# Kernel tuning notes

Measured on AMD Instinct MI355X. Metric: run time of the kernel, lower is better.

Reference implementation:

```python
import jax, jax.numpy as jnp
import numpy as np

B, T, D, F, C = 32768, 256, 10, 512, 1  # batch, trees, max_depth, features, classes
LVL_PAD = T * 2 ** (D - 1)  # padded width of per-level node/bias tables


def setup_inputs() -> dict:
    key = jax.random.key(0)
    k = jax.random.split(key, 6)
    x = jax.random.normal(k[0], (B, F), dtype=jnp.float32)
    root_nodes = jax.random.randint(k[1], (T,), 0, F, dtype=jnp.int32)
    root_biases = jax.random.normal(k[2], (T,), dtype=jnp.float32)
    # levels 1..D-1 packed into a padded matrix; level i uses first T*2**i entries
    nodes = jax.random.randint(k[3], (D - 1, LVL_PAD), 0, F, dtype=jnp.int32)
    biases = jax.random.normal(k[4], (D - 1, LVL_PAD), dtype=jnp.float32)
    leaf_nodes = jax.random.normal(k[5], (T * 2 ** D, C), dtype=jnp.float32)
    return {"x": x, "root_nodes": root_nodes, "root_biases": root_biases,
            "nodes": nodes, "biases": biases, "leaf_nodes": leaf_nodes}


def reference(x, root_nodes, root_biases, nodes, biases, leaf_nodes):
    b = x.shape[0]
    t = root_nodes.shape[0]
    depth = nodes.shape[0] + 1
    tree_indices = 2 * jnp.arange(t, dtype=jnp.int32)  # [T]
    # root level: cond(x[:, root_nodes], root_biases) -> child index offset per tree
    prev = (x[:, root_nodes] <= root_biases).astype(jnp.int32) + tree_indices  # [B, T]
    prev = prev.reshape(-1)  # [B*T]
    for i in range(1, depth):
        width = t * (2 ** i)
        lvl_nodes = nodes[i - 1, :width]    # [T*2^i]
        lvl_biases = biases[i - 1, :width]  # [T*2^i]
        gather_idx = lvl_nodes[prev].reshape(b, t)              # [B, T] feature ids
        feats = jnp.take_along_axis(x, gather_idx, axis=1).reshape(-1)  # [B*T]
        cond = (feats <= lvl_biases[prev]).astype(jnp.int32)
        prev = 2 * prev + cond
    out = leaf_nodes[prev].reshape(b, t, -1)  # [B, T, C]
    return out
```

## Files before the change

kernel.cpp:

```cpp
#include <hip/hip_runtime.h>

constexpr int kB = 32768;
constexpr int kT = 256;
constexpr int kD = 10;
constexpr int kF = 512;
constexpr int kLvlPad = kT << (kD - 1);
constexpr int kLevels = kD - 1;

constexpr int kRows    = 16;
constexpr int kTrees   = 128;
constexpr int kChains  = 4;
constexpr int kThreads = 512;
constexpr int kXPad    = 516;
constexpr int kOPad    = kTrees + 1;

constexpr int kP1 = kT * 2;
constexpr int kP3 = kT * 8;
constexpr int kP5 = kT * 32;
constexpr int kP7 = kT * 128;
constexpr int kFU = kT * 512;
constexpr int kO1 = 0;
constexpr int kO3 = kO1 + kP1;
constexpr int kO5 = kO3 + kP3;
constexpr int kO7 = kO5 + kP5;
constexpr int kOF = kO7 + kP7;
constexpr int kTotalRecs = kOF + kFU;
constexpr size_t kWsBytes = (size_t)kTotalRecs * 16;

__global__ __launch_bounds__(256)
void prep_kernel(const int* __restrict__ nodes, const float* __restrict__ biases,
                 const float* __restrict__ leaf_nodes, int4* __restrict__ ws)
{
    int idx = blockIdx.x * 256 + threadIdx.x;
    if (idx < kOF) {
        int i, base;
        if      (idx < kO3) { i = 1; base = kO1; }
        else if (idx < kO5) { i = 3; base = kO3; }
        else if (idx < kO7) { i = 5; base = kO5; }
        else                { i = 7; base = kO7; }
        int j = idx - base;
        const int*   nt = nodes  + (size_t)(i - 1) * kLvlPad;
        const float* bt = biases + (size_t)(i - 1) * kLvlPad;
        const int*   nc = nodes  + (size_t)i * kLvlPad;
        const float* bc = biases + (size_t)i * kLvlPad;
        unsigned int pk = (unsigned int)nt[j]
                        | ((unsigned int)nc[2 * j]     << 9)
                        | ((unsigned int)nc[2 * j + 1] << 18);
        ws[idx] = make_int4((int)pk, __float_as_int(bt[j]),
                            __float_as_int(bc[2 * j]),
                            __float_as_int(bc[2 * j + 1]));
    } else if (idx < kTotalRecs) {
        int j = idx - kOF;
        const int   n9 = nodes [(size_t)(kD - 2) * kLvlPad + j];
        const float b9 = biases[(size_t)(kD - 2) * kLvlPad + j];
        ws[idx] = make_int4(n9, __float_as_int(b9),
                            __float_as_int(leaf_nodes[2 * j]),
                            __float_as_int(leaf_nodes[2 * j + 1]));
    }
}

__global__ __launch_bounds__(kThreads)
void traverse_pair_kernel(const float* __restrict__ x,
                          const int* __restrict__ root_nodes,
                          const float* __restrict__ root_biases,
                          const int4* __restrict__ ws,
                          float* __restrict__ out)
{
    __shared__ float xs[kRows][kXPad];
    float* outs = &xs[0][0];

    const int bid = blockIdx.x;
    const int w   = bid >> 4;
    const int s   = bid & 15;
    const int bx  = w * 8 + (s & 7);
    const int by  = s >> 3;
    const int b0  = bx * kRows;
    const int t0  = by * kTrees;
    const int tid = threadIdx.x;

    {
        const float4* xg = reinterpret_cast<const float4*>(x + (size_t)b0 * kF);
#pragma unroll
        for (int k = 0; k < 4; ++k) {
            int j = tid + k * kThreads;
            int r = j >> 7;
            int c = j & 127;
            float4 v = xg[(size_t)r * (kF / 4) + c];
            *reinterpret_cast<float4*>(&xs[r][c * 4]) = v;
        }
    }
    __syncthreads();

    const int r  = tid & (kRows - 1);
    const int tt = tid >> 4;
    const float* __restrict__ xrow = xs[r];

    int p[kChains];
#pragma unroll
    for (int c = 0; c < kChains; ++c) {
        int t = t0 + tt + 32 * c;
        p[c] = 2 * t + (xrow[root_nodes[t]] <= root_biases[t] ? 1 : 0);
    }

    const int4* __restrict__ P1 = ws + kO1;
    const int4* __restrict__ P3 = ws + kO3;
    const int4* __restrict__ P5 = ws + kO5;
    const int4* __restrict__ P7 = ws + kO7;
    const int4* __restrict__ FU = ws + kOF;

#define PAIR_STEP(TBL)                                                        \
    {                                                                         \
        int4 rec[kChains];                                                    \
        _Pragma("unroll")                                                     \
        for (int c = 0; c < kChains; ++c) rec[c] = TBL[p[c]];                 \
        _Pragma("unroll")                                                     \
        for (int c = 0; c < kChains; ++c) {                                   \
            unsigned int n = (unsigned int)rec[c].x;                          \
            int c0 = xrow[n & 511u] <= __int_as_float(rec[c].y) ? 1 : 0;      \
            int nc = c0 ? (int)((n >> 18) & 511u) : (int)((n >> 9) & 511u);   \
            int bb = c0 ? rec[c].w : rec[c].z;                                \
            int c1 = xrow[nc] <= __int_as_float(bb) ? 1 : 0;                  \
            p[c] = 4 * p[c] + 2 * c0 + c1;                                    \
        }                                                                     \
    }

    PAIR_STEP(P1)
    PAIR_STEP(P3)
    PAIR_STEP(P5)
    PAIR_STEP(P7)
#undef PAIR_STEP

    float leaf[kChains];
    {
        int4 rec[kChains];
#pragma unroll
        for (int c = 0; c < kChains; ++c) rec[c] = FU[p[c]];
#pragma unroll
        for (int c = 0; c < kChains; ++c) {
            leaf[c] = __int_as_float(
                xrow[rec[c].x] <= __int_as_float(rec[c].y) ? rec[c].w
                                                           : rec[c].z);
        }
    }

    __syncthreads();
#pragma unroll
    for (int c = 0; c < kChains; ++c)
        outs[r * kOPad + tt + 32 * c] = leaf[c];
    __syncthreads();

#pragma unroll
    for (int k = 0; k < 4; ++k) {
        int j    = tid + k * kThreads;
        int orow = j >> 7;
        int ocol = j & 127;
        __builtin_nontemporal_store(outs[orow * kOPad + ocol],
                                    &out[(size_t)(b0 + orow) * kT + t0 + ocol]);
    }
}

__global__ __launch_bounds__(kThreads)
void traverse_plain_kernel(const float* __restrict__ x,
                           const int* __restrict__ root_nodes,
                           const float* __restrict__ root_biases,
                           const int* __restrict__ nodes,
                           const float* __restrict__ biases,
                           const float* __restrict__ leaf_nodes,
                           float* __restrict__ out)
{
    __shared__ float xs[kRows][kXPad];
    __shared__ float outs[kRows][65];

    const int b0  = blockIdx.x * kRows;
    const int t0  = blockIdx.y * 64;
    const int tid = threadIdx.x;

    {
        const float4* xg = reinterpret_cast<const float4*>(x + (size_t)b0 * kF);
#pragma unroll
        for (int k = 0; k < 4; ++k) {
            int j = tid + k * kThreads;
            int r = j >> 7;
            int c = j & 127;
            float4 v = xg[(size_t)r * (kF / 4) + c];
            *reinterpret_cast<float4*>(&xs[r][c * 4]) = v;
        }
    }
    __syncthreads();

    const int r  = tid & (kRows - 1);
    const int tt = tid >> 4;
    const int tA = t0 + tt;
    const int tB = t0 + tt + 32;
    const float* __restrict__ xrow = xs[r];

    int pA = 2 * tA + (xrow[root_nodes[tA]] <= root_biases[tA] ? 1 : 0);
    int pB = 2 * tB + (xrow[root_nodes[tB]] <= root_biases[tB] ? 1 : 0);

#pragma unroll
    for (int i = 1; i < kD; ++i) {
        const int*   ln = nodes  + (size_t)(i - 1) * kLvlPad;
        const float* lb = biases + (size_t)(i - 1) * kLvlPad;
        int   nA = ln[pA], nB = ln[pB];
        float bA = lb[pA], bB = lb[pB];
        pA = 2 * pA + (xrow[nA] <= bA ? 1 : 0);
        pB = 2 * pB + (xrow[nB] <= bB ? 1 : 0);
    }

    outs[r][tt]      = leaf_nodes[pA];
    outs[r][tt + 32] = leaf_nodes[pB];
    __syncthreads();

#pragma unroll
    for (int k = 0; k < 2; ++k) {
        int j    = tid + k * kThreads;
        int orow = j >> 6;
        int ocol = j & 63;
        __builtin_nontemporal_store(outs[orow][ocol],
                                    &out[(size_t)(b0 + orow) * kT + t0 + ocol]);
    }
}

extern "C" void kernel_launch(void* const* d_in, const int* in_sizes, int n_in,
                              void* d_out, int out_size, void* d_ws, size_t ws_size,
                              hipStream_t stream) {
    const float* x           = (const float*)d_in[0];
    const int*   root_nodes  = (const int*)d_in[1];
    const float* root_biases = (const float*)d_in[2];
    const int*   nodes       = (const int*)d_in[3];
    const float* biases      = (const float*)d_in[4];
    const float* leaf_nodes  = (const float*)d_in[5];
    float*       out         = (float*)d_out;

    if (ws_size >= kWsBytes) {
        prep_kernel<<<(kTotalRecs + 255) / 256, 256, 0, stream>>>(
            nodes, biases, leaf_nodes, (int4*)d_ws);
        const int nblocks = (kB / kRows) * (kT / kTrees);
        traverse_pair_kernel<<<nblocks, kThreads, 0, stream>>>(
            x, root_nodes, root_biases, (const int4*)d_ws, out);
    } else {
        dim3 grid(kB / kRows, kT / 64);
        traverse_plain_kernel<<<grid, kThreads, 0, stream>>>(
            x, root_nodes, root_biases, nodes, biases, leaf_nodes, out);
    }
}
```

Before: 67.36 us.

## Retile pair traversal to 64 rows by 64 trees and prefetch both child features

The pair-traversal kernel now uses 1024-thread blocks covering 64 batch rows and 64 trees, where it previously used 16 rows and 128 trees. A wavefront now spans 64 rows of one tree, so each node-table record load is shared across the whole wave instead of being scattered over many trees. Each pair step also reads both candidate child features from LDS before the first compare is resolved, which removes the dependent LDS load at the cost of one extra read. Each block stages 64 x rows (about 132 KB of LDS), which may limit occupancy to one block per CU. The x tile is now also reloaded once per 64-tree group rather than once per 128-tree group.

```diff
diff --git a/kernel.cpp b/kernel.cpp
--- a/kernel.cpp
+++ b/kernel.cpp
@@ -7,12 +7,12 @@
 constexpr int kLvlPad = kT << (kD - 1);
 constexpr int kLevels = kD - 1;
 
-constexpr int kRows    = 16;
-constexpr int kTrees   = 128;
+constexpr int kRows    = 64;
+constexpr int kTreesPB = 64;
 constexpr int kChains  = 4;
-constexpr int kThreads = 512;
+constexpr int kThreads = 1024;
 constexpr int kXPad    = 516;
-constexpr int kOPad    = kTrees + 1;
+constexpr int kOPad    = 65;
 
 constexpr int kP1 = kT * 2;
 constexpr int kP3 = kT * 8;
@@ -70,18 +70,18 @@
     float* outs = &xs[0][0];
 
     const int bid = blockIdx.x;
-    const int w   = bid >> 4;
-    const int s   = bid & 15;
+    const int w   = bid >> 5;
+    const int s   = bid & 31;
     const int bx  = w * 8 + (s & 7);
     const int by  = s >> 3;
     const int b0  = bx * kRows;
-    const int t0  = by * kTrees;
+    const int t0  = by * kTreesPB;
     const int tid = threadIdx.x;
 
     {
         const float4* xg = reinterpret_cast<const float4*>(x + (size_t)b0 * kF);
 #pragma unroll
-        for (int k = 0; k < 4; ++k) {
+        for (int k = 0; k < 8; ++k) {
             int j = tid + k * kThreads;
             int r = j >> 7;
             int c = j & 127;
@@ -91,14 +91,14 @@
     }
     __syncthreads();
 
-    const int r  = tid & (kRows - 1);
-    const int tt = tid >> 4;
+    const int r    = tid & (kRows - 1);
+    const int slot = tid >> 6;
     const float* __restrict__ xrow = xs[r];
 
     int p[kChains];
 #pragma unroll
     for (int c = 0; c < kChains; ++c) {
-        int t = t0 + tt + 32 * c;
+        int t = t0 + slot + 16 * c;
         p[c] = 2 * t + (xrow[root_nodes[t]] <= root_biases[t] ? 1 : 0);
     }
 
@@ -116,10 +116,13 @@
         _Pragma("unroll")                                                     \
         for (int c = 0; c < kChains; ++c) {                                   \
             unsigned int n = (unsigned int)rec[c].x;                          \
-            int c0 = xrow[n & 511u] <= __int_as_float(rec[c].y) ? 1 : 0;      \
-            int nc = c0 ? (int)((n >> 18) & 511u) : (int)((n >> 9) & 511u);   \
-            int bb = c0 ? rec[c].w : rec[c].z;                                \
-            int c1 = xrow[nc] <= __int_as_float(bb) ? 1 : 0;                  \
+            float ft = xrow[n & 511u];                                        \
+            float fl = xrow[(n >> 9) & 511u];                                 \
+            float fr = xrow[(n >> 18) & 511u];                                \
+            int c0 = ft <= __int_as_float(rec[c].y) ? 1 : 0;                  \
+            float fc = c0 ? fr : fl;                                          \
+            int   bb = c0 ? rec[c].w : rec[c].z;                              \
+            int c1 = fc <= __int_as_float(bb) ? 1 : 0;                        \
             p[c] = 4 * p[c] + 2 * c0 + c1;                                    \
         }                                                                     \
     }
@@ -146,20 +149,20 @@
     __syncthreads();
 #pragma unroll
     for (int c = 0; c < kChains; ++c)
-        outs[r * kOPad + tt + 32 * c] = leaf[c];
+        outs[r * kOPad + slot + 16 * c] = leaf[c];
     __syncthreads();
 
 #pragma unroll
     for (int k = 0; k < 4; ++k) {
         int j    = tid + k * kThreads;
-        int orow = j >> 7;
-        int ocol = j & 127;
+        int orow = j >> 6;
+        int ocol = j & 63;
         __builtin_nontemporal_store(outs[orow * kOPad + ocol],
                                     &out[(size_t)(b0 + orow) * kT + t0 + ocol]);
     }
 }
 
-__global__ __launch_bounds__(kThreads)
+__global__ __launch_bounds__(512)
 void traverse_plain_kernel(const float* __restrict__ x,
                            const int* __restrict__ root_nodes,
                            const float* __restrict__ root_biases,
@@ -168,10 +171,10 @@
                            const float* __restrict__ leaf_nodes,
                            float* __restrict__ out)
 {
-    __shared__ float xs[kRows][kXPad];
-    __shared__ float outs[kRows][65];
-
-    const int b0  = blockIdx.x * kRows;
+    __shared__ float xs[16][kXPad];
+    __shared__ float outs[16][65];
+
+    const int b0  = blockIdx.x * 16;
     const int t0  = blockIdx.y * 64;
     const int tid = threadIdx.x;
 
@@ -179,7 +182,7 @@
         const float4* xg = reinterpret_cast<const float4*>(x + (size_t)b0 * kF);
 #pragma unroll
         for (int k = 0; k < 4; ++k) {
-            int j = tid + k * kThreads;
+            int j = tid + k * 512;
             int r = j >> 7;
             int c = j & 127;
             float4 v = xg[(size_t)r * (kF / 4) + c];
@@ -188,7 +191,7 @@
     }
     __syncthreads();
 
-    const int r  = tid & (kRows - 1);
+    const int r  = tid & 15;
     const int tt = tid >> 4;
     const int tA = t0 + tt;
     const int tB = t0 + tt + 32;
@@ -213,7 +216,7 @@
 
 #pragma unroll
     for (int k = 0; k < 2; ++k) {
-        int j    = tid + k * kThreads;
+        int j    = tid + k * 512;
         int orow = j >> 6;
         int ocol = j & 63;
         __builtin_nontemporal_store(outs[orow][ocol],
@@ -235,12 +238,12 @@
     if (ws_size >= kWsBytes) {
         prep_kernel<<<(kTotalRecs + 255) / 256, 256, 0, stream>>>(
             nodes, biases, leaf_nodes, (int4*)d_ws);
-        const int nblocks = (kB / kRows) * (kT / kTrees);
+        const int nblocks = (kB / kRows) * (kT / kTreesPB);
         traverse_pair_kernel<<<nblocks, kThreads, 0, stream>>>(
             x, root_nodes, root_biases, (const int4*)d_ws, out);
     } else {
-        dim3 grid(kB / kRows, kT / 64);
-        traverse_plain_kernel<<<grid, kThreads, 0, stream>>>(
+        dim3 grid(kB / 16, kT / 64);
+        traverse_plain_kernel<<<grid, 512, 0, stream>>>(
             x, root_nodes, root_biases, nodes, biases, leaf_nodes, out);
     }
 }
```

Result: no change. 68.05 us (+1.0%).

## Re-pair tree levels from the root and pack the last two levels with leaves

Applied to the files above, without the earlier changes.

The precomputed node tables are now paired starting at the root (levels 0-1, 2-3, 4-5, 6-7). The final block packs levels 8-9 plus four leaf values into two 16-byte records per node. This removes the separate root-node gather and the single-level final step, so each thread does five dependent gather rounds instead of six. In exchange the final table is twice as large (32 bytes per entry) and each thread needs more registers to hold two records per chain.

```diff
diff --git a/kernel.cpp b/kernel.cpp
--- a/kernel.cpp
+++ b/kernel.cpp
@@ -5,7 +5,6 @@
 constexpr int kD = 10;
 constexpr int kF = 512;
 constexpr int kLvlPad = kT << (kD - 1);
-constexpr int kLevels = kD - 1;
 
 constexpr int kRows    = 16;
 constexpr int kTrees   = 128;
@@ -14,55 +13,69 @@
 constexpr int kXPad    = 516;
 constexpr int kOPad    = kTrees + 1;
 
-constexpr int kP1 = kT * 2;
-constexpr int kP3 = kT * 8;
-constexpr int kP5 = kT * 32;
-constexpr int kP7 = kT * 128;
-constexpr int kFU = kT * 512;
-constexpr int kO1 = 0;
-constexpr int kO3 = kO1 + kP1;
-constexpr int kO5 = kO3 + kP3;
-constexpr int kO7 = kO5 + kP5;
-constexpr int kOF = kO7 + kP7;
-constexpr int kTotalRecs = kOF + kFU;
-constexpr size_t kWsBytes = (size_t)kTotalRecs * 16;
+constexpr int kN01 = 256;
+constexpr int kN23 = 1024;
+constexpr int kN45 = 4096;
+constexpr int kN67 = 16384;
+constexpr int kNF  = 65536;
+constexpr int kO01 = 0;
+constexpr int kO23 = kO01 + kN01;
+constexpr int kO45 = kO23 + kN23;
+constexpr int kO67 = kO45 + kN45;
+constexpr int kOFU = kO67 + kN67;
+constexpr int kPairTotal = kOFU;
+constexpr int kPrepThreads = kPairTotal + kNF;
+constexpr size_t kWsBytes = (size_t)(kOFU + 2 * kNF) * 16;
 
 __global__ __launch_bounds__(256)
-void prep_kernel(const int* __restrict__ nodes, const float* __restrict__ biases,
+void prep_kernel(const int* __restrict__ root_nodes,
+                 const float* __restrict__ root_biases,
+                 const int* __restrict__ nodes, const float* __restrict__ biases,
                  const float* __restrict__ leaf_nodes, int4* __restrict__ ws)
 {
     int idx = blockIdx.x * 256 + threadIdx.x;
-    if (idx < kOF) {
-        int i, base;
-        if      (idx < kO3) { i = 1; base = kO1; }
-        else if (idx < kO5) { i = 3; base = kO3; }
-        else if (idx < kO7) { i = 5; base = kO5; }
-        else                { i = 7; base = kO7; }
-        int j = idx - base;
-        const int*   nt = nodes  + (size_t)(i - 1) * kLvlPad;
-        const float* bt = biases + (size_t)(i - 1) * kLvlPad;
-        const int*   nc = nodes  + (size_t)i * kLvlPad;
-        const float* bc = biases + (size_t)i * kLvlPad;
-        unsigned int pk = (unsigned int)nt[j]
+    if (idx < kPairTotal) {
+        int j, topL;
+        if      (idx < kO23) { topL = 0; j = idx - kO01; }
+        else if (idx < kO45) { topL = 2; j = idx - kO23; }
+        else if (idx < kO67) { topL = 4; j = idx - kO45; }
+        else                 { topL = 6; j = idx - kO67; }
+        int   nt; float bt;
+        if (topL == 0) { nt = root_nodes[j]; bt = root_biases[j]; }
+        else {
+            nt = nodes [(size_t)(topL - 1) * kLvlPad + j];
+            bt = biases[(size_t)(topL - 1) * kLvlPad + j];
+        }
+        const int*   nc = nodes  + (size_t)topL * kLvlPad;
+        const float* bc = biases + (size_t)topL * kLvlPad;
+        unsigned int pk = (unsigned int)nt
                         | ((unsigned int)nc[2 * j]     << 9)
                         | ((unsigned int)nc[2 * j + 1] << 18);
-        ws[idx] = make_int4((int)pk, __float_as_int(bt[j]),
+        ws[idx] = make_int4((int)pk, __float_as_int(bt),
                             __float_as_int(bc[2 * j]),
                             __float_as_int(bc[2 * j + 1]));
-    } else if (idx < kTotalRecs) {
-        int j = idx - kOF;
-        const int   n9 = nodes [(size_t)(kD - 2) * kLvlPad + j];
-        const float b9 = biases[(size_t)(kD - 2) * kLvlPad + j];
-        ws[idx] = make_int4(n9, __float_as_int(b9),
-                            __float_as_int(leaf_nodes[2 * j]),
-                            __float_as_int(leaf_nodes[2 * j + 1]));
+    } else if (idx < kPrepThreads) {
+        int j = idx - kPairTotal;
+        const int   n8 = nodes [(size_t)7 * kLvlPad + j];
+        const float b8 = biases[(size_t)7 * kLvlPad + j];
+        const int*   n9 = nodes  + (size_t)8 * kLvlPad;
+        const float* b9 = biases + (size_t)8 * kLvlPad;
+        unsigned int pk = (unsigned int)n8
+                        | ((unsigned int)n9[2 * j]     << 9)
+                        | ((unsigned int)n9[2 * j + 1] << 18);
+        ws[kOFU + 2 * j] = make_int4((int)pk, __float_as_int(b8),
+                                     __float_as_int(b9[2 * j]),
+                                     __float_as_int(b9[2 * j + 1]));
+        ws[kOFU + 2 * j + 1] =
+            make_int4(__float_as_int(leaf_nodes[4 * j]),
+                      __float_as_int(leaf_nodes[4 * j + 1]),
+                      __float_as_int(leaf_nodes[4 * j + 2]),
+                      __float_as_int(leaf_nodes[4 * j + 3]));
     }
 }
 
 __global__ __launch_bounds__(kThreads)
 void traverse_pair_kernel(const float* __restrict__ x,
-                          const int* __restrict__ root_nodes,
-                          const float* __restrict__ root_biases,
                           const int4* __restrict__ ws,
                           float* __restrict__ out)
 {
@@ -95,18 +108,16 @@
     const int tt = tid >> 4;
     const float* __restrict__ xrow = xs[r];
 
+    const int4* __restrict__ P01 = ws + kO01;
+    const int4* __restrict__ P23 = ws + kO23;
+    const int4* __restrict__ P45 = ws + kO45;
+    const int4* __restrict__ P67 = ws + kO67;
+    const int4* __restrict__ FU  = ws + kOFU;
+
     int p[kChains];
 #pragma unroll
-    for (int c = 0; c < kChains; ++c) {
-        int t = t0 + tt + 32 * c;
-        p[c] = 2 * t + (xrow[root_nodes[t]] <= root_biases[t] ? 1 : 0);
-    }
-
-    const int4* __restrict__ P1 = ws + kO1;
-    const int4* __restrict__ P3 = ws + kO3;
-    const int4* __restrict__ P5 = ws + kO5;
-    const int4* __restrict__ P7 = ws + kO7;
-    const int4* __restrict__ FU = ws + kOF;
+    for (int c = 0; c < kChains; ++c)
+        p[c] = t0 + tt + 32 * c;
 
 #define PAIR_STEP(TBL)                                                        \
     {                                                                         \
@@ -124,22 +135,30 @@
         }                                                                     \
     }
 
-    PAIR_STEP(P1)
-    PAIR_STEP(P3)
-    PAIR_STEP(P5)
-    PAIR_STEP(P7)
+    PAIR_STEP(P01)
+    PAIR_STEP(P23)
+    PAIR_STEP(P45)
+    PAIR_STEP(P67)
 #undef PAIR_STEP
 
     float leaf[kChains];
     {
-        int4 rec[kChains];
-#pragma unroll
-        for (int c = 0; c < kChains; ++c) rec[c] = FU[p[c]];
+        int4 lo[kChains], hi[kChains];
 #pragma unroll
         for (int c = 0; c < kChains; ++c) {
-            leaf[c] = __int_as_float(
-                xrow[rec[c].x] <= __int_as_float(rec[c].y) ? rec[c].w
-                                                           : rec[c].z);
+            lo[c] = FU[2 * p[c]];
+            hi[c] = FU[2 * p[c] + 1];
+        }
+#pragma unroll
+        for (int c = 0; c < kChains; ++c) {
+            unsigned int n = (unsigned int)lo[c].x;
+            int c8 = xrow[n & 511u] <= __int_as_float(lo[c].y) ? 1 : 0;
+            int n9 = c8 ? (int)((n >> 18) & 511u) : (int)((n >> 9) & 511u);
+            int b9 = c8 ? lo[c].w : lo[c].z;
+            int c9 = xrow[n9] <= __int_as_float(b9) ? 1 : 0;
+            int lv = c8 ? (c9 ? hi[c].w : hi[c].z)
+                        : (c9 ? hi[c].y : hi[c].x);
+            leaf[c] = __int_as_float(lv);
         }
     }
 
@@ -159,7 +178,7 @@
     }
 }
 
-__global__ __launch_bounds__(kThreads)
+__global__ __launch_bounds__(512)
 void traverse_plain_kernel(const float* __restrict__ x,
                            const int* __restrict__ root_nodes,
                            const float* __restrict__ root_biases,
@@ -168,10 +187,10 @@
                            const float* __restrict__ leaf_nodes,
                            float* __restrict__ out)
 {
-    __shared__ float xs[kRows][kXPad];
-    __shared__ float outs[kRows][65];
-
-    const int b0  = blockIdx.x * kRows;
+    __shared__ float xs[16][kXPad];
+    __shared__ float outs[16][65];
+
+    const int b0  = blockIdx.x * 16;
     const int t0  = blockIdx.y * 64;
     const int tid = threadIdx.x;
 
@@ -179,7 +198,7 @@
         const float4* xg = reinterpret_cast<const float4*>(x + (size_t)b0 * kF);
 #pragma unroll
         for (int k = 0; k < 4; ++k) {
-            int j = tid + k * kThreads;
+            int j = tid + k * 512;
             int r = j >> 7;
             int c = j & 127;
             float4 v = xg[(size_t)r * (kF / 4) + c];
@@ -188,7 +207,7 @@
     }
     __syncthreads();
 
-    const int r  = tid & (kRows - 1);
+    const int r  = tid & 15;
     const int tt = tid >> 4;
     const int tA = t0 + tt;
     const int tB = t0 + tt + 32;
@@ -213,7 +232,7 @@
 
 #pragma unroll
     for (int k = 0; k < 2; ++k) {
-        int j    = tid + k * kThreads;
+        int j    = tid + k * 512;
         int orow = j >> 6;
         int ocol = j & 63;
         __builtin_nontemporal_store(outs[orow][ocol],
@@ -233,14 +252,14 @@
     float*       out         = (float*)d_out;
 
     if (ws_size >= kWsBytes) {
-        prep_kernel<<<(kTotalRecs + 255) / 256, 256, 0, stream>>>(
-            nodes, biases, leaf_nodes, (int4*)d_ws);
+        prep_kernel<<<(kPrepThreads + 255) / 256, 256, 0, stream>>>(
+            root_nodes, root_biases, nodes, biases, leaf_nodes, (int4*)d_ws);
         const int nblocks = (kB / kRows) * (kT / kTrees);
         traverse_pair_kernel<<<nblocks, kThreads, 0, stream>>>(
-            x, root_nodes, root_biases, (const int4*)d_ws, out);
+            x, (const int4*)d_ws, out);
     } else {
-        dim3 grid(kB / kRows, kT / 64);
-        traverse_plain_kernel<<<grid, kThreads, 0, stream>>>(
+        dim3 grid(kB / 16, kT / 64);
+        traverse_plain_kernel<<<grid, 512, 0, stream>>>(
             x, root_nodes, root_biases, nodes, biases, leaf_nodes, out);
     }
 }
```

After: 73.94 us. 1.1x slower.
